# Kernel tuning notes

Measured on AMD Instinct MI355X. Metric: run time of the kernel, lower is better.

Reference implementation:

```python
import jax, jax.numpy as jnp
from jax import lax
import numpy as np

B, T, D, H, DH, FF, K = 16, 1024, 512, 8, 64, 2048, 3
EPS = 1e-5


def _layer_norm(x, g, b):
    mu = jnp.mean(x, axis=-1, keepdims=True)
    var = jnp.mean((x - mu) ** 2, axis=-1, keepdims=True)
    return (x - mu) / jnp.sqrt(var + EPS) * g + b


def setup_inputs() -> dict:
    key = jax.random.key(0)
    ks = jax.random.split(key, 14)
    f32 = jnp.float32
    dec_inp = jax.random.normal(ks[0], (B, T, D), f32)
    lengths = jax.random.randint(ks[1], (B,), T // 2, T + 1)
    mask = (jnp.arange(T)[None, :] < lengths[:, None])[:, :, None]  # [B,T,1] bool
    qkv_w = jax.random.normal(ks[2], (3 * H * DH, D), f32) * (D ** -0.5)
    qkv_b = jnp.zeros((3 * H * DH,), f32)
    o_w = jax.random.normal(ks[3], (D, H * DH), f32) * ((H * DH) ** -0.5)
    ln1_g = jnp.ones((D,), f32)
    ln1_b = jnp.zeros((D,), f32)
    conv1_w = jax.random.normal(ks[4], (FF, D, K), f32) * ((D * K) ** -0.5)
    conv1_b = jnp.zeros((FF,), f32)
    conv2_w = jax.random.normal(ks[5], (D, FF, K), f32) * ((FF * K) ** -0.5)
    conv2_b = jnp.zeros((D,), f32)
    ln2_g = jnp.ones((D,), f32)
    ln2_b = jnp.zeros((D,), f32)
    return dict(dec_inp=dec_inp, mask=mask, qkv_w=qkv_w, qkv_b=qkv_b, o_w=o_w,
                ln1_g=ln1_g, ln1_b=ln1_b, conv1_w=conv1_w, conv1_b=conv1_b,
                conv2_w=conv2_w, conv2_b=conv2_b, ln2_g=ln2_g, ln2_b=ln2_b)


def reference(dec_inp, mask, qkv_w, qkv_b, o_w, ln1_g, ln1_b,
              conv1_w, conv1_b, conv2_w, conv2_b, ln2_g, ln2_b):
    # ----- MultiHeadAttn (post-norm, dropout = identity in eval) -----
    attn_mask = ~mask[:, :, 0]                      # [B,T], True = pad
    qkv = dec_inp @ qkv_w.T + qkv_b                 # [B,T,3*H*DH]
    q, k, v = jnp.split(qkv, 3, axis=2)

    def to_heads(x):  # [B,T,H*DH] -> [B*H,T,DH] (batch-major, as in torch)
        return x.reshape(B, T, H, DH).transpose(0, 2, 1, 3).reshape(B * H, T, DH)

    q, k, v = to_heads(q), to_heads(k), to_heads(v)
    scores = jnp.einsum('bqd,bkd->bqk', q, k) * (DH ** -0.5)  # [B*H,T,T]
    # faithful to torch: mask tiled head-major (index i % B)
    am = jnp.tile(attn_mask[:, None, :], (H, T, 1))           # [B*H,T,T]
    scores = jnp.where(am, -jnp.inf, scores)
    prob = jax.nn.softmax(scores, axis=2)
    vec = jnp.einsum('bqk,bkd->bqd', prob, v)                 # [B*H,T,DH]
    # faithful to torch: view as [H,B,...] then permute
    vec = vec.reshape(H, B, T, DH).transpose(1, 2, 0, 3).reshape(B, T, H * DH)
    attn_out = vec @ o_w.T                                    # [B,T,D]
    out = _layer_norm(dec_inp + attn_out, ln1_g, ln1_b)
    out = out * mask

    # ----- PositionwiseConvFF (post-norm) -----
    x = out.transpose(0, 2, 1)                                # [B,D,T]
    h = lax.conv_general_dilated(x, conv1_w, (1,), [(K // 2, K // 2)],
                                 dimension_numbers=('NCH', 'OIH', 'NCH'))
    h = jax.nn.relu(h + conv1_b[None, :, None])
    h = lax.conv_general_dilated(h, conv2_w, (1,), [(K // 2, K // 2)],
                                 dimension_numbers=('NCH', 'OIH', 'NCH'))
    core = (h + conv2_b[None, :, None]).transpose(0, 2, 1)    # [B,T,D]
    out = _layer_norm(out + core, ln2_g, ln2_b)
    return out * mask
```

## Files before the change

kernel.cpp:

```cpp
#include <hip/hip_runtime.h>

using h16 = _Float16;
using h16x4 = __attribute__((ext_vector_type(4))) _Float16;
using h16x8 = __attribute__((ext_vector_type(8))) _Float16;
using f32x4 = __attribute__((ext_vector_type(4))) float;

static constexpr int cB = 16, cT = 1024, cD = 512, cH = 8, cDH = 64, cFF = 2048;
static constexpr int cM = cB * cT;
static constexpr int cTP = cT + 2;

__device__ __forceinline__ bool mask_val(const void* mb, int idx) {
  const unsigned char* u8 = (const unsigned char*)mb;
  if (u8[1] == 1) return u8[idx] != 0;
  const float* f = (const float*)mb;
  if (f[1] == 1.0f) return f[idx] != 0.0f;
  return ((const int*)mb)[idx] != 0;
}

__device__ __forceinline__ void gl_lds16(const h16* g, h16* l) {
  __builtin_amdgcn_global_load_lds(
      (const __attribute__((address_space(1))) unsigned int*)g,
      (__attribute__((address_space(3))) unsigned int*)l, 16, 0, 0);
}


__global__ __launch_bounds__(256) void k_cast4(const float* __restrict__ in,
                                               h16* __restrict__ out, int n4) {
  int i = blockIdx.x * 256 + threadIdx.x;
  if (i >= n4) return;
  const float4 f = ((const float4*)in)[i];
  h16x4 o = {(h16)f.x, (h16)f.y, (h16)f.z, (h16)f.w};
  ((h16x4*)out)[i] = o;
}

__global__ __launch_bounds__(256) void k_repack_w1(const float* __restrict__ w,
                                                   h16* __restrict__ out) {
  int i = blockIdx.x * 256 + threadIdx.x;
  if (i >= cFF * cD) return;
  int f = i >> 9, d = i & 511;
#pragma unroll
  for (int k = 0; k < 3; ++k)
    out[f * (3 * cD) + k * cD + d] = (h16)w[(long)i * 3 + k];
}

__global__ __launch_bounds__(256) void k_repack_w2(const float* __restrict__ w,
                                                   h16* __restrict__ out) {
  int i = blockIdx.x * 256 + threadIdx.x;
  if (i >= cD * cFF) return;
  int o = i >> 11, f = i & 2047;
#pragma unroll
  for (int k = 0; k < 3; ++k)
    out[o * (3 * cFF) + k * cFF + f] = (h16)w[(long)i * 3 + k];
}

__global__ __launch_bounds__(256) void k_zero_pads(h16* __restrict__ xp,
                                                   h16* __restrict__ hp) {
  int i = blockIdx.x * 256 + threadIdx.x;
  if (i < cB * 2 * cD) {
    int b = i / (2 * cD); int rr = (i / cD) & 1; int c = i % cD;
    xp[((long)b * cTP + rr * (cTP - 1)) * cD + c] = (h16)0.f;
  }
  if (i < cB * 2 * cFF) {
    int b = i / (2 * cFF); int rr = (i / cFF) & 1; int c = i % cFF;
    hp[((long)b * cTP + rr * (cTP - 1)) * cFF + c] = (h16)0.f;
  }
}

template <int SKIP, bool A_CONV, bool OUT_CONV, bool BIAS, bool RELU,
          bool OUT_H16, bool VSCAT, int SPLITK, bool SWIZ>
__global__ __launch_bounds__(256)
void gemm_bt(const h16* __restrict__ A, const h16* __restrict__ W,
             const float* __restrict__ bias, void* __restrict__ Cv,
             h16* __restrict__ Vg, const void* __restrict__ maskbuf,
             int ldc, int Kd, int lda, long zstride) {
  __shared__ h16 smem[2 * 128 * 64];
  h16* As = smem;
  h16* Bs = smem + 128 * 64;
  const int tid = threadIdx.x;
  const int w = tid >> 6, l = tid & 63;
  int m0, n0;
  if (SWIZ) {
    m0 = (blockIdx.x * 16 + (blockIdx.y >> 2)) * 128;
    n0 = (blockIdx.y & 3) * 128;
  } else {
    m0 = blockIdx.y * 128;
    n0 = blockIdx.x * 128;
  }

  if (SKIP == 1) {
    if (!mask_val(maskbuf, m0)) return;
  } else if (SKIP == 2) {
    int t0 = m0 & 1023, base = ((m0 >> 10) & 1) * 8;
    bool need = false;
#pragma unroll
    for (int i = 0; i < 8; ++i) need |= mask_val(maskbuf, ((base + i) << 10) + t0);
    if (!need) return;
  } else if (SKIP == 3) {
    int t0 = m0 & 1023;
    if (t0 && !mask_val(maskbuf, m0 - 1)) return;
  }

  const int wm = (w >> 1) * 64, wn = (w & 1) * 64;
  const int lr = l >> 3;
  const int lcs = ((l & 7) ^ lr) * 8;
  const int fr = l & 15;
  const int fb = fr & 7;
  const int qd = l >> 4;

  const int kspan = (SPLITK == 2) ? (Kd >> 1) : Kd;
  const int kbeg = (SPLITK == 2) ? blockIdx.z * kspan : 0;
  const int kend = kbeg + kspan;

  f32x4 zero4 = {0.f, 0.f, 0.f, 0.f};
  f32x4 acc[4][4];
#pragma unroll
  for (int mi = 0; mi < 4; ++mi)
#pragma unroll
    for (int ni = 0; ni < 4; ++ni) acc[mi][ni] = zero4;

  for (int k0 = kbeg; k0 < kend; k0 += 64) {
    __syncthreads();
#pragma unroll
    for (int i = 0; i < 4; ++i) {
      int c = w * 4 + i;
      int ar = m0 + c * 8 + lr;
      long aoff = (long)(ar + (A_CONV ? 2 * (ar >> 10) : 0)) * lda + k0 + lcs;
      gl_lds16(A + aoff, &As[c * 512]);
      int br = n0 + c * 8 + lr;
      long boff = (long)br * Kd + k0 + lcs;
      gl_lds16(W + boff, &Bs[c * 512]);
    }
    __syncthreads();
#pragma unroll
    for (int kc = 0; kc < 2; ++kc) {
      h16x8 af[4], bfr[4];
#pragma unroll
      for (int mi = 0; mi < 4; ++mi)
        af[mi] = *(const h16x8*)&As[(wm + mi * 16 + fr) * 64 +
                                    (((kc * 4 + qd) ^ fb) * 8)];
#pragma unroll
      for (int ni = 0; ni < 4; ++ni)
        bfr[ni] = *(const h16x8*)&Bs[(wn + ni * 16 + fr) * 64 +
                                     (((kc * 4 + qd) ^ fb) * 8)];
#pragma unroll
      for (int mi = 0; mi < 4; ++mi)
#pragma unroll
        for (int ni = 0; ni < 4; ++ni)
          acc[mi][ni] = __builtin_amdgcn_mfma_f32_16x16x32_f16(
              af[mi], bfr[ni], acc[mi][ni], 0, 0, 0);
    }
  }
  const bool do_bias = BIAS && (SPLITK == 1 || blockIdx.z == 0);
  if (VSCAT && n0 >= 1024) {
#pragma unroll
    for (int mi = 0; mi < 4; ++mi) {
      int t0 = (m0 + wm + mi * 16 + (l >> 4) * 4) & 1023;
      int jj = ((m0 >> 10) << 3);
#pragma unroll
      for (int ni = 0; ni < 4; ++ni) {
        int gc = n0 + wn + ni * 16 + fr;
        int dh = gc & 63;
        int j2 = jj + ((gc - 1024) >> 6);
        float bb = do_bias ? bias[gc] : 0.f;
        h16x4 v4 = {(h16)(acc[mi][ni][0] + bb), (h16)(acc[mi][ni][1] + bb),
                    (h16)(acc[mi][ni][2] + bb), (h16)(acc[mi][ni][3] + bb)};
        *(h16x4*)&Vg[((long)j2 * 64 + dh) * 1024 + t0] = v4;
      }
    }
  } else if (OUT_H16) {
    __syncthreads();
#pragma unroll
    for (int mi = 0; mi < 4; ++mi) {
#pragma unroll
      for (int ni = 0; ni < 4; ++ni) {
#pragma unroll
        for (int rr = 0; rr < 4; ++rr) {
          int rrow = wm + mi * 16 + (l >> 4) * 4 + rr;
          int ccol = wn + ni * 16 + fr;
          float v = acc[mi][ni][rr];
          if (do_bias) v += bias[n0 + ccol];
          if (RELU) v = v > 0.f ? v : 0.f;
          smem[rrow * 128 + ccol] = (h16)v;
        }
      }
    }
    __syncthreads();
    h16* outp = (h16*)Cv + (SPLITK == 2 ? (long)blockIdx.z * zstride : 0);
    const int r2 = tid >> 4, c2 = (tid & 15) * 8;
#pragma unroll
    for (int i = 0; i < 8; ++i) {
      int row = r2 + i * 16;
      int gr = m0 + row;
      long orow = (long)gr + (OUT_CONV ? (2 * (gr >> 10) + 1) : 0);
      *(h16x8*)&outp[orow * ldc + n0 + c2] = *(h16x8*)&smem[row * 128 + c2];
    }
  } else {
#pragma unroll
    for (int mi = 0; mi < 4; ++mi) {
#pragma unroll
      for (int ni = 0; ni < 4; ++ni) {
#pragma unroll
        for (int rr = 0; rr < 4; ++rr) {
          int gr = m0 + wm + mi * 16 + (l >> 4) * 4 + rr;
          int gc = n0 + wn + ni * 16 + fr;
          float v = acc[mi][ni][rr];
          if (do_bias) v += bias[gc];
          if (RELU) v = v > 0.f ? v : 0.f;
          long orow = (long)gr + (OUT_CONV ? (2 * (gr >> 10) + 1) : 0);
          ((float*)Cv)[orow * ldc + gc] = v;
        }
      }
    }
  }
}

template <int SKIP, bool A_CONV, bool OUT_CONV, bool BIAS, bool RELU,
          int SPLITK, int NBLK_LOG2>
__global__ __launch_bounds__(1024, 4)
void gemm16(const h16* __restrict__ A, const h16* __restrict__ W,
            const float* __restrict__ bias, h16* __restrict__ C,
            const void* __restrict__ maskbuf, int ldc, int Kd, int lda,
            long zstride) {
  extern __shared__ h16 sm[];
  const int tid = threadIdx.x;
  const int wid = tid >> 6, l = tid & 63;
  const int m0 = (blockIdx.x * 8 + (blockIdx.y >> NBLK_LOG2)) * 256;
  const int n0 = (blockIdx.y & ((1 << NBLK_LOG2) - 1)) * 256;

  if (SKIP == 1) {
    if (!mask_val(maskbuf, m0)) return;
  } else if (SKIP == 3) {
    int t0 = m0 & 1023;
    if (t0 && !mask_val(maskbuf, m0 - 1)) return;
  }

  const int wm = wid >> 2, wn = wid & 3;
  const int fr = l & 15, qd = l >> 4;

  const int kspan = (SPLITK == 2) ? (Kd >> 1) : Kd;
  const int kbeg = (SPLITK == 2) ? blockIdx.z * kspan : 0;
  const int nt = kspan >> 5;

  f32x4 zero4 = {0.f, 0.f, 0.f, 0.f};
  f32x4 acc[4][4];
#pragma unroll
  for (int m = 0; m < 4; ++m)
#pragma unroll
    for (int n = 0; n < 4; ++n) acc[m][n] = zero4;

  const int srow = tid >> 2;
  const int sch = ((tid & 3) - ((tid >> 3) & 3)) & 3;
  const int ar0 = m0 + srow;
  const long aoff0 =
      (long)(ar0 + (A_CONV ? 2 * (ar0 >> 10) : 0)) * lda + kbeg + sch * 8;
  const long boff0 = (long)(n0 + srow) * Kd + kbeg + sch * 8;
  auto stage = [&](int ti) {
    h16* buf = sm + (ti & 3) * 16384;
    gl_lds16(A + aoff0 + ti * 32, &buf[wid * 512]);
    gl_lds16(W + boff0 + ti * 32, &buf[8192 + wid * 512]);
  };

  const int abase = (wm * 64 + fr) * 32 + (((qd + (fr >> 1)) & 3) * 8);
  const int bbase = (wn * 64 + fr) * 32 + (((qd + (fr >> 1)) & 3) * 8);

  stage(0);
  if (nt > 1) stage(1);
  asm volatile("s_waitcnt vmcnt(0)" ::: "memory");
  __builtin_amdgcn_s_barrier();

  for (int s = 0; s < nt; s += 2) {
    if (s + 2 < nt) stage(s + 2);
    if (s + 3 < nt) stage(s + 3);
#pragma unroll
    for (int u = 0; u < 2; ++u) {
      const int t = s + u;
      const h16* Ab = sm + (t & 3) * 16384;
      const h16* Bb = Ab + 8192;
      h16x8 a[4], b[4];
#pragma unroll
      for (int m = 0; m < 4; ++m)
        a[m] = *(const h16x8*)&Ab[abase + m * 512];
#pragma unroll
      for (int n = 0; n < 4; ++n)
        b[n] = *(const h16x8*)&Bb[bbase + n * 512];
      __builtin_amdgcn_s_setprio(1);
#pragma unroll
      for (int m = 0; m < 4; ++m)
#pragma unroll
        for (int n = 0; n < 4; ++n)
          acc[m][n] = __builtin_amdgcn_mfma_f32_16x16x32_f16(a[m], b[n],
                                                             acc[m][n], 0, 0, 0);
      __builtin_amdgcn_s_setprio(0);
    }
    asm volatile("s_waitcnt vmcnt(0)" ::: "memory");
    __builtin_amdgcn_s_barrier();
  }

  const bool do_bias = BIAS && (SPLITK == 1 || blockIdx.z == 0);
  const int qd4 = qd * 4;
#pragma unroll
  for (int m = 0; m < 4; ++m) {
    int row = wm * 64 + m * 16 + qd4;
#pragma unroll
    for (int n = 0; n < 4; ++n) {
      int col = wn * 64 + n * 16 + fr;
      float bb = do_bias ? bias[n0 + col] : 0.f;
#pragma unroll
      for (int rr = 0; rr < 4; ++rr) {
        float v = acc[m][n][rr] + bb;
        if (RELU) v = v > 0.f ? v : 0.f;
        sm[(row + rr) * 256 + col] = (h16)v;
      }
    }
  }
  __syncthreads();
  h16* outp = C + (SPLITK == 2 ? (long)blockIdx.z * zstride : 0);
  const int r2 = tid >> 5, c2 = (tid & 31) * 8;
#pragma unroll
  for (int i = 0; i < 8; ++i) {
    int row = r2 + i * 32;
    int gr = m0 + row;
    long orow = (long)gr + (OUT_CONV ? (2 * (gr >> 10) + 1) : 0);
    *(h16x8*)&outp[orow * (long)ldc + n0 + c2] = *(h16x8*)&sm[row * 256 + c2];
  }
}

__global__ __launch_bounds__(256)
void k_attn(const h16* __restrict__ qk, const h16* __restrict__ Vg,
            const void* __restrict__ maskbuf, h16* __restrict__ attn_out) {
  __shared__ h16 Ks[2][64 * 64];
  __shared__ h16 Vt[2][64 * 64];
  __shared__ h16 Ps[4][16 * 68];
  __shared__ float sbias[2][64];
  const int tid = threadIdx.x, w = tid >> 6, l = tid & 63;
  const int f = blockIdx.x;
  const int bp = f & 15, qt = (f >> 4) & 15, hp = f >> 8;
  const int j = hp * 16 + bp;
  const int bd = j >> 3, hd = j & 7;

  if (!mask_val(maskbuf, bp * cT + qt * 64)) return;

  const int fr = l & 15, fq = (l >> 4) * 8;
  const int fb = fr & 7, qd = l >> 4;
  const int lr = l >> 3, lcs = ((l & 7) ^ lr) * 8;

  int nkv = 16;
  for (int t = 8; t < 16; ++t)
    if (!mask_val(maskbuf, bp * cT + t * 64)) { nkv = t; break; }

  h16x8 qf[2];
#pragma unroll
  for (int kc = 0; kc < 2; ++kc) {
    qf[kc] = *(const h16x8*)&qk[
        (long)((bd << 10) + qt * 64 + w * 16 + fr) * 1024 +
        hd * 64 + kc * 32 + fq];
    qf[kc] *= (h16)0.125f;
  }

  auto stageKV = [&](int t) {
    const int buf = t & 1;
    const int k0 = t * 64;
#pragma unroll
    for (int i = 0; i < 2; ++i) {
      int c = w * 2 + i;
      int row = c * 8 + lr;
      gl_lds16(qk + (long)((bd << 10) + k0 + row) * 1024 + 512 + hd * 64 + lcs,
               &Ks[buf][c * 512]);
      gl_lds16(Vg + ((long)j * 64 + row) * 1024 + k0 + lcs, &Vt[buf][c * 512]);
    }
    if (tid < 64)
      sbias[buf][tid] = mask_val(maskbuf, bp * cT + k0 + tid) ? 0.f : -1e30f;
  };

  f32x4 zero4 = {0.f, 0.f, 0.f, 0.f};
  f32x4 o[4];
  float lrow[4];
#pragma unroll
  for (int nt = 0; nt < 4; ++nt) o[nt] = zero4;
#pragma unroll
  for (int r = 0; r < 4; ++r) lrow[r] = 0.f;

  stageKV(0);
  __syncthreads();

  for (int t = 0; t < nkv; ++t) {
    const int cur = t & 1;
    if (t + 1 < nkv) stageKV(t + 1);

    f32x4 S[4];
#pragma unroll
    for (int kt = 0; kt < 4; ++kt) {
      float sb = sbias[cur][kt * 16 + fr];
      f32x4 s = {sb, sb, sb, sb};
#pragma unroll
      for (int kc = 0; kc < 2; ++kc) {
        h16x8 kf = *(const h16x8*)&Ks[cur][(kt * 16 + fr) * 64 +
                                          (((kc * 4 + qd) ^ fb) * 8)];
        s = __builtin_amdgcn_mfma_f32_16x16x32_f16(qf[kc], kf, s, 0, 0, 0);
      }
      S[kt] = s;
    }
#pragma unroll
    for (int r = 0; r < 4; ++r) {
      float p0 = __expf(S[0][r] - 4.f), p1 = __expf(S[1][r] - 4.f);
      float p2 = __expf(S[2][r] - 4.f), p3 = __expf(S[3][r] - 4.f);
      lrow[r] += (p0 + p1) + (p2 + p3);
      int ql = (l >> 4) * 4 + r;
      Ps[w][ql * 68 + fr] = (h16)p0;
      Ps[w][ql * 68 + 16 + fr] = (h16)p1;
      Ps[w][ql * 68 + 32 + fr] = (h16)p2;
      Ps[w][ql * 68 + 48 + fr] = (h16)p3;
    }
#pragma unroll
    for (int kp = 0; kp < 2; ++kp) {
      h16x8 pf = *(const h16x8*)&Ps[w][fr * 68 + kp * 32 + fq];
#pragma unroll
      for (int nt = 0; nt < 4; ++nt) {
        h16x8 vf = *(const h16x8*)&Vt[cur][(nt * 16 + fr) * 64 +
                                           (((kp * 4 + qd) ^ fb) * 8)];
        o[nt] = __builtin_amdgcn_mfma_f32_16x16x32_f16(pf, vf, o[nt], 0, 0, 0);
      }
    }
    __syncthreads();
  }
#pragma unroll
  for (int r = 0; r < 4; ++r) {
#pragma unroll
    for (int m = 1; m < 16; m <<= 1) lrow[r] += __shfl_xor(lrow[r], m);
    float inv = 1.f / lrow[r];
    int q = qt * 64 + w * 16 + (l >> 4) * 4 + r;
    long row = (long)bp * cT + q;
#pragma unroll
    for (int nt = 0; nt < 4; ++nt)
      attn_out[row * cD + hp * 64 + nt * 16 + fr] = (h16)(o[nt][r] * inv);
  }
}

template <bool WRITE_XP, bool RH16, bool R2H16, bool XH16, bool WRITE_OUTF>
__global__ __launch_bounds__(256)
void k_ln(const void* __restrict__ Xv, const void* __restrict__ Rv,
          const void* __restrict__ Rv2,
          const float* __restrict__ g, const float* __restrict__ bta,
          const void* __restrict__ maskbuf,
          float* __restrict__ outf, h16* __restrict__ xp) {
  const int w = threadIdx.x >> 6, l = threadIdx.x & 63;
  const long row = (long)blockIdx.x * 4 + w;
  float v[8];
  if (XH16) {
    const long xr = row + 2 * (row >> 10) + 1;
    const h16x4* x4 = (const h16x4*)((const h16*)Xv + xr * cD);
    h16x4 a0 = x4[l], a1 = x4[l + 64];
    v[0] = (float)a0[0]; v[1] = (float)a0[1];
    v[2] = (float)a0[2]; v[3] = (float)a0[3];
    v[4] = (float)a1[0]; v[5] = (float)a1[1];
    v[6] = (float)a1[2]; v[7] = (float)a1[3];
  } else {
    const float4* x4 = (const float4*)((const float*)Xv + row * cD);
    float4 a0 = x4[l], a1 = x4[l + 64];
    v[0] = a0.x; v[1] = a0.y; v[2] = a0.z; v[3] = a0.w;
    v[4] = a1.x; v[5] = a1.y; v[6] = a1.z; v[7] = a1.w;
  }
  if (RH16) {
    const h16x4* r4 = (const h16x4*)((const h16*)Rv + row * cD);
    h16x4 b0 = r4[l], b1 = r4[l + 64];
    v[0] += (float)b0[0]; v[1] += (float)b0[1];
    v[2] += (float)b0[2]; v[3] += (float)b0[3];
    v[4] += (float)b1[0]; v[5] += (float)b1[1];
    v[6] += (float)b1[2]; v[7] += (float)b1[3];
  } else {
    const float4* r4 = (const float4*)((const float*)Rv + row * cD);
    float4 b0 = r4[l], b1 = r4[l + 64];
    v[0] += b0.x; v[1] += b0.y; v[2] += b0.z; v[3] += b0.w;
    v[4] += b1.x; v[5] += b1.y; v[6] += b1.z; v[7] += b1.w;
  }
  if (R2H16) {
    const h16x4* r4 = (const h16x4*)((const h16*)Rv2 + row * cD);
    h16x4 b0 = r4[l], b1 = r4[l + 64];
    v[0] += (float)b0[0]; v[1] += (float)b0[1];
    v[2] += (float)b0[2]; v[3] += (float)b0[3];
    v[4] += (float)b1[0]; v[5] += (float)b1[1];
    v[6] += (float)b1[2]; v[7] += (float)b1[3];
  }
  float s = 0.f;
#pragma unroll
  for (int i = 0; i < 8; ++i) s += v[i];
#pragma unroll
  for (int m = 1; m < 64; m <<= 1) s += __shfl_xor(s, m);
  const float mu = s * (1.f / 512.f);
  float s2 = 0.f;
#pragma unroll
  for (int i = 0; i < 8; ++i) { float d = v[i] - mu; s2 += d * d; }
#pragma unroll
  for (int m = 1; m < 64; m <<= 1) s2 += __shfl_xor(s2, m);
  const float rstd = rsqrtf(s2 * (1.f / 512.f) + 1e-5f);
  const float mv = mask_val(maskbuf, (int)row) ? 1.f : 0.f;
  const float4* g4 = (const float4*)g;
  const float4* t4 = (const float4*)bta;
  float4 g0 = g4[l], g1 = g4[l + 64], t0 = t4[l], t1 = t4[l + 64];
  float4 y0, y1;
  y0.x = ((v[0] - mu) * rstd * g0.x + t0.x) * mv;
  y0.y = ((v[1] - mu) * rstd * g0.y + t0.y) * mv;
  y0.z = ((v[2] - mu) * rstd * g0.z + t0.z) * mv;
  y0.w = ((v[3] - mu) * rstd * g0.w + t0.w) * mv;
  y1.x = ((v[4] - mu) * rstd * g1.x + t1.x) * mv;
  y1.y = ((v[5] - mu) * rstd * g1.y + t1.y) * mv;
  y1.z = ((v[6] - mu) * rstd * g1.z + t1.z) * mv;
  y1.w = ((v[7] - mu) * rstd * g1.w + t1.w) * mv;
  if (WRITE_OUTF) {
    ((float4*)(outf + row * cD))[l] = y0;
    ((float4*)(outf + row * cD))[l + 64] = y1;
  }
  if (WRITE_XP) {
    const long xrow = row + 2 * (row >> 10) + 1;
    h16x4 h0 = {(h16)y0.x, (h16)y0.y, (h16)y0.z, (h16)y0.w};
    h16x4 h1 = {(h16)y1.x, (h16)y1.y, (h16)y1.z, (h16)y1.w};
    ((h16x4*)(xp + xrow * cD))[l] = h0;
    ((h16x4*)(xp + xrow * cD))[l + 64] = h1;
  }
}

extern "C" void kernel_launch(void* const* d_in, const int* in_sizes, int n_in,
                              void* d_out, int out_size, void* d_ws, size_t ws_size,
                              hipStream_t stream) {
  const float* dec   = (const float*)d_in[0];
  const void*  maskb = d_in[1];
  const float* qkv_w = (const float*)d_in[2];
  const float* qkv_b = (const float*)d_in[3];
  const float* o_w   = (const float*)d_in[4];
  const float* ln1g  = (const float*)d_in[5];
  const float* ln1b  = (const float*)d_in[6];
  const float* c1w   = (const float*)d_in[7];
  const float* c1b   = (const float*)d_in[8];
  const float* c2w   = (const float*)d_in[9];
  const float* c2b   = (const float*)d_in[10];
  const float* ln2g  = (const float*)d_in[11];
  const float* ln2b  = (const float*)d_in[12];

  char* p = (char*)d_ws;
  auto alloc = [&](size_t bytes) {
    char* r = p; p += (bytes + 255) & ~(size_t)255; return r;
  };
  h16*   dec_h  = (h16*)alloc((size_t)cM * cD * 2);
  h16*   qkvw_h = (h16*)alloc((size_t)1536 * cD * 2);
  h16*   ow_h   = (h16*)alloc((size_t)cD * cD * 2);
  h16*   w1p    = (h16*)alloc((size_t)cFF * 3 * cD * 2);
  h16*   w2p    = (h16*)alloc((size_t)cD * 3 * cFF * 2);
  h16*   qk_h   = (h16*)alloc((size_t)cM * 1024 * 2);
  h16*   vg     = (h16*)alloc((size_t)cB * cH * cDH * cT * 2);
  h16*   attn_h = (h16*)alloc((size_t)cM * cD * 2);
  float* tmp    = (float*)alloc((size_t)cM * cD * 4);
  float* out1   = (float*)alloc((size_t)cM * cD * 4);
  h16*   xp     = (h16*)alloc((size_t)cB * cTP * cD * 2);
  h16*   hp     = (h16*)alloc((size_t)cB * cTP * cFF * 2);
  h16*   core0 = attn_h;
  h16*   core1 = qk_h;
  h16*   tmp_h = (h16*)tmp;
  (void)ws_size; (void)n_in; (void)in_sizes; (void)out_size; (void)out1;

  static bool s_attr = false;
  if (!s_attr) {
    hipFuncSetAttribute(
        reinterpret_cast<const void*>(&gemm16<3, true, true, true, true, 1, 3>),
        hipFuncAttributeMaxDynamicSharedMemorySize, 131072);
    hipFuncSetAttribute(
        reinterpret_cast<const void*>(&gemm16<1, true, false, true, false, 2, 1>),
        hipFuncAttributeMaxDynamicSharedMemorySize, 131072);
    s_attr = true;
  }

  k_cast4<<<(cM * cD / 4 + 255) / 256, 256, 0, stream>>>(dec, dec_h, cM * cD / 4);
  k_cast4<<<(1536 * cD / 4 + 255) / 256, 256, 0, stream>>>(qkv_w, qkvw_h, 1536 * cD / 4);
  k_cast4<<<(cD * cD / 4 + 255) / 256, 256, 0, stream>>>(o_w, ow_h, cD * cD / 4);
  k_repack_w1<<<(cFF * cD + 255) / 256, 256, 0, stream>>>(c1w, w1p);
  k_repack_w2<<<(cD * cFF + 255) / 256, 256, 0, stream>>>(c2w, w2p);
  k_zero_pads<<<(cB * 2 * cFF + 255) / 256, 256, 0, stream>>>(xp, hp);

  gemm_bt<2, false, false, true, false, true, true, 1, false>
      <<<dim3(12, cM / 128), 256, 0, stream>>>(dec_h, qkvw_h, qkv_b, qk_h, vg,
                                               maskb, 1024, cD, cD, 0);

  k_attn<<<dim3(2048), 256, 0, stream>>>(qk_h, vg, maskb, attn_h);

  gemm_bt<1, false, false, false, false, true, false, 1, false>
      <<<dim3(cD / 128, cM / 128), 256, 0, stream>>>(attn_h, ow_h, nullptr, tmp_h,
                                                     nullptr, maskb, cD, cD, cD, 0);

  k_ln<true, true, false, false, false><<<cM / 4, 256, 0, stream>>>(
      dec, tmp_h, nullptr, ln1g, ln1b, maskb, nullptr, xp);

  gemm16<3, true, true, true, true, 1, 3>
      <<<dim3(8, 64), dim3(1024), 131072, stream>>>(xp, w1p, c1b, hp, maskb,
                                                    cFF, 3 * cD, cD, 0);

  gemm16<1, true, false, true, false, 2, 1>
      <<<dim3(8, 16, 2), dim3(1024), 131072, stream>>>(hp, w2p, c2b, core0,
                                                       maskb, cD, 3 * cFF, cFF,
                                                       (long)(core1 - core0));

  k_ln<false, true, true, true, true><<<cM / 4, 256, 0, stream>>>(
      xp, core0, core1, ln2g, ln2b, maskb, (float*)d_out, nullptr);
}
```

Before: 482.8 us.

## Merge prep kernels into one launch and widen attention tiles to 128 queries

The six preprocessing launches (input and weight casts, conv weight repacks, pad zeroing) become a single kernel that picks its job from block-index ranges, removing launch overhead. The attention kernel now uses 512 threads, so each block handles 128 query rows with 8 waves and the K/V tiles staged in shared memory are reused across twice as many queries. Fewer blocks means less parallelism per CU, and the early exit now tests masking at 128-row granularity, so more fully padded rows get computed. The key-tile loop bound still uses the first padded 64-row tile.

After: 455.5 us. 1.06x faster.

```diff
diff --git a/kernel.cpp b/kernel.cpp
--- a/kernel.cpp
+++ b/kernel.cpp
@@ -24,45 +24,51 @@
 }
 
 
-__global__ __launch_bounds__(256) void k_cast4(const float* __restrict__ in,
-                                               h16* __restrict__ out, int n4) {
-  int i = blockIdx.x * 256 + threadIdx.x;
-  if (i >= n4) return;
-  const float4 f = ((const float4*)in)[i];
-  h16x4 o = {(h16)f.x, (h16)f.y, (h16)f.z, (h16)f.w};
-  ((h16x4*)out)[i] = o;
-}
-
-__global__ __launch_bounds__(256) void k_repack_w1(const float* __restrict__ w,
-                                                   h16* __restrict__ out) {
-  int i = blockIdx.x * 256 + threadIdx.x;
-  if (i >= cFF * cD) return;
-  int f = i >> 9, d = i & 511;
-#pragma unroll
-  for (int k = 0; k < 3; ++k)
-    out[f * (3 * cD) + k * cD + d] = (h16)w[(long)i * 3 + k];
-}
-
-__global__ __launch_bounds__(256) void k_repack_w2(const float* __restrict__ w,
-                                                   h16* __restrict__ out) {
-  int i = blockIdx.x * 256 + threadIdx.x;
-  if (i >= cD * cFF) return;
-  int o = i >> 11, f = i & 2047;
-#pragma unroll
-  for (int k = 0; k < 3; ++k)
-    out[o * (3 * cFF) + k * cFF + f] = (h16)w[(long)i * 3 + k];
-}
-
-__global__ __launch_bounds__(256) void k_zero_pads(h16* __restrict__ xp,
-                                                   h16* __restrict__ hp) {
-  int i = blockIdx.x * 256 + threadIdx.x;
-  if (i < cB * 2 * cD) {
-    int b = i / (2 * cD); int rr = (i / cD) & 1; int c = i % cD;
-    xp[((long)b * cTP + rr * (cTP - 1)) * cD + c] = (h16)0.f;
-  }
-  if (i < cB * 2 * cFF) {
-    int b = i / (2 * cFF); int rr = (i / cFF) & 1; int c = i % cFF;
-    hp[((long)b * cTP + rr * (cTP - 1)) * cFF + c] = (h16)0.f;
+__global__ __launch_bounds__(256)
+void k_prep(const float* __restrict__ dec, h16* __restrict__ dec_h,
+            const float* __restrict__ qkv_w, h16* __restrict__ qkvw_h,
+            const float* __restrict__ o_w, h16* __restrict__ ow_h,
+            const float* __restrict__ c1w, h16* __restrict__ w1p,
+            const float* __restrict__ c2w, h16* __restrict__ w2p,
+            h16* __restrict__ xp, h16* __restrict__ hp) {
+  const int b = blockIdx.x;
+  if (b < 8192) {
+    int i = b * 256 + threadIdx.x;
+    const float4 f = ((const float4*)dec)[i];
+    h16x4 o = {(h16)f.x, (h16)f.y, (h16)f.z, (h16)f.w};
+    ((h16x4*)dec_h)[i] = o;
+  } else if (b < 8960) {
+    int i = (b - 8192) * 256 + threadIdx.x;
+    const float4 f = ((const float4*)qkv_w)[i];
+    h16x4 o = {(h16)f.x, (h16)f.y, (h16)f.z, (h16)f.w};
+    ((h16x4*)qkvw_h)[i] = o;
+  } else if (b < 9216) {
+    int i = (b - 8960) * 256 + threadIdx.x;
+    const float4 f = ((const float4*)o_w)[i];
+    h16x4 o = {(h16)f.x, (h16)f.y, (h16)f.z, (h16)f.w};
+    ((h16x4*)ow_h)[i] = o;
+  } else if (b < 13312) {
+    int i = (b - 9216) * 256 + threadIdx.x;
+    int f = i >> 9, d = i & 511;
+#pragma unroll
+    for (int k = 0; k < 3; ++k)
+      w1p[f * (3 * cD) + k * cD + d] = (h16)c1w[(long)i * 3 + k];
+  } else if (b < 17408) {
+    int i = (b - 13312) * 256 + threadIdx.x;
+    int o = i >> 11, f = i & 2047;
+#pragma unroll
+    for (int k = 0; k < 3; ++k)
+      w2p[o * (3 * cFF) + k * cFF + f] = (h16)c2w[(long)i * 3 + k];
+  } else {
+    int i = (b - 17408) * 256 + threadIdx.x;
+    if (i < cB * 2 * cD) {
+      int bb = i / (2 * cD); int rr = (i / cD) & 1; int c = i % cD;
+      xp[((long)bb * cTP + rr * (cTP - 1)) * cD + c] = (h16)0.f;
+    }
+    if (i < cB * 2 * cFF) {
+      int bb = i / (2 * cFF); int rr = (i / cFF) & 1; int c = i % cFF;
+      hp[((long)bb * cTP + rr * (cTP - 1)) * cFF + c] = (h16)0.f;
+    }
   }
 }
 
@@ -325,20 +331,20 @@
   }
 }
 
-__global__ __launch_bounds__(256)
+__global__ __launch_bounds__(512, 6)
 void k_attn(const h16* __restrict__ qk, const h16* __restrict__ Vg,
             const void* __restrict__ maskbuf, h16* __restrict__ attn_out) {
   __shared__ h16 Ks[2][64 * 64];
   __shared__ h16 Vt[2][64 * 64];
-  __shared__ h16 Ps[4][16 * 68];
+  __shared__ h16 Ps[8][16 * 68];
   __shared__ float sbias[2][64];
   const int tid = threadIdx.x, w = tid >> 6, l = tid & 63;
   const int f = blockIdx.x;
-  const int bp = f & 15, qt = (f >> 4) & 15, hp = f >> 8;
+  const int bp = f & 15, qt = (f >> 4) & 7, hp = f >> 7;
   const int j = hp * 16 + bp;
   const int bd = j >> 3, hd = j & 7;
 
-  if (!mask_val(maskbuf, bp * cT + qt * 64)) return;
+  if (!mask_val(maskbuf, bp * cT + qt * 128)) return;
 
   const int fr = l & 15, fq = (l >> 4) * 8;
   const int fb = fr & 7, qd = l >> 4;
@@ -352,7 +358,7 @@
 #pragma unroll
   for (int kc = 0; kc < 2; ++kc) {
     qf[kc] = *(const h16x8*)&qk[
-        (long)((bd << 10) + qt * 64 + w * 16 + fr) * 1024 +
+        (long)((bd << 10) + qt * 128 + w * 16 + fr) * 1024 +
         hd * 64 + kc * 32 + fq];
     qf[kc] *= (h16)0.125f;
   }
@@ -360,14 +366,11 @@
   auto stageKV = [&](int t) {
     const int buf = t & 1;
     const int k0 = t * 64;
-#pragma unroll
-    for (int i = 0; i < 2; ++i) {
-      int c = w * 2 + i;
-      int row = c * 8 + lr;
-      gl_lds16(qk + (long)((bd << 10) + k0 + row) * 1024 + 512 + hd * 64 + lcs,
-               &Ks[buf][c * 512]);
-      gl_lds16(Vg + ((long)j * 64 + row) * 1024 + k0 + lcs, &Vt[buf][c * 512]);
-    }
+    const int c = w;
+    const int row = c * 8 + lr;
+    gl_lds16(qk + (long)((bd << 10) + k0 + row) * 1024 + 512 + hd * 64 + lcs,
+             &Ks[buf][c * 512]);
+    gl_lds16(Vg + ((long)j * 64 + row) * 1024 + k0 + lcs, &Vt[buf][c * 512]);
     if (tid < 64)
       sbias[buf][tid] = mask_val(maskbuf, bp * cT + k0 + tid) ? 0.f : -1e30f;
   };
@@ -428,7 +431,7 @@
 #pragma unroll
     for (int m = 1; m < 16; m <<= 1) lrow[r] += __shfl_xor(lrow[r], m);
     float inv = 1.f / lrow[r];
-    int q = qt * 64 + w * 16 + (l >> 4) * 4 + r;
+    int q = qt * 128 + w * 16 + (l >> 4) * 4 + r;
     long row = (long)bp * cT + q;
 #pragma unroll
     for (int nt = 0; nt < 4; ++nt)
@@ -568,18 +571,14 @@
     s_attr = true;
   }
 
-  k_cast4<<<(cM * cD / 4 + 255) / 256, 256, 0, stream>>>(dec, dec_h, cM * cD / 4);
-  k_cast4<<<(1536 * cD / 4 + 255) / 256, 256, 0, stream>>>(qkv_w, qkvw_h, 1536 * cD / 4);
-  k_cast4<<<(cD * cD / 4 + 255) / 256, 256, 0, stream>>>(o_w, ow_h, cD * cD / 4);
-  k_repack_w1<<<(cFF * cD + 255) / 256, 256, 0, stream>>>(c1w, w1p);
-  k_repack_w2<<<(cD * cFF + 255) / 256, 256, 0, stream>>>(c2w, w2p);
-  k_zero_pads<<<(cB * 2 * cFF + 255) / 256, 256, 0, stream>>>(xp, hp);
+  k_prep<<<dim3(17664), 256, 0, stream>>>(dec, dec_h, qkv_w, qkvw_h, o_w, ow_h,
+                                          c1w, w1p, c2w, w2p, xp, hp);
 
   gemm_bt<2, false, false, true, false, true, true, 1, false>
       <<<dim3(12, cM / 128), 256, 0, stream>>>(dec_h, qkvw_h, qkv_b, qk_h, vg,
                                                maskb, 1024, cD, cD, 0);
 
-  k_attn<<<dim3(2048), 256, 0, stream>>>(qk_h, vg, maskb, attn_h);
+  k_attn<<<dim3(1024), 512, 0, stream>>>(qk_h, vg, maskb, attn_h);
 
   gemm_bt<1, false, false, false, false, true, false, 1, false>
       <<<dim3(cD / 128, cM / 128), 256, 0, stream>>>(attn_h, ow_h, nullptr, tmp_h,
```
